# Optimization experiments

Measured on AMD Instinct MI355X. Metric: run time of the kernel, lower is better.

The kernel has to match this reference:

```python
import jax, jax.numpy as jnp
import numpy as np

S = 2048      # words in the sentence
LMAX = 16     # max chars per word (padded)
VOCAB = 50000
ALPHA = 256
CE = 256      # char_embedding_dim (also char-LSTM hidden)
WE = 512      # word_embedding_dim
H = 1024      # hidden_dim of word LSTM


def setup_inputs() -> dict:
    key = jax.random.key(0)
    ks = jax.random.split(key, 13)
    def u(k, shape, scale):
        return jax.random.uniform(k, shape, jnp.float32, -scale, scale)
    sc_c = 1.0 / np.sqrt(CE).astype(np.float32)   # torch LSTM init scale
    sc_w = 1.0 / np.sqrt(H).astype(np.float32)
    return {
        "word_idxs": jax.random.randint(ks[0], (S,), 0, VOCAB),
        "char_idxs": jax.random.randint(ks[1], (S, LMAX), 0, ALPHA),
        "char_lens": jax.random.randint(ks[2], (S,), 1, LMAX + 1),
        "char_emb": jax.random.normal(ks[3], (ALPHA, CE), jnp.float32) * 0.1,
        "word_emb": jax.random.normal(ks[4], (VOCAB, WE), jnp.float32) * 0.1,
        "Wih_c": u(ks[5], (4 * CE, CE), sc_c),
        "Whh_c": u(ks[6], (4 * CE, CE), sc_c),
        "bih_c": u(ks[7], (4 * CE,), sc_c),
        "bhh_c": u(ks[8], (4 * CE,), sc_c),
        "Wih_w": u(ks[9], (4 * H, WE + CE), sc_w),
        "Whh_w": u(ks[10], (4 * H, H), sc_w),
        "bih_w": u(ks[11], (4 * H,), sc_w),
        "bhh_w": u(ks[12], (4 * H,), sc_w),
    }


def _lstm_scan(xs, Wih, Whh, bih, bhh, hdim):
    """Single-layer LSTM, torch gate order (i, f, g, o). xs: [T, B, D] -> hs [T, B, hdim]."""
    B = xs.shape[1]
    bias = bih + bhh
    def step(carry, x):
        h, c = carry
        gates = x @ Wih.T + h @ Whh.T + bias  # [B, 4*hdim]
        i, f, g, o = jnp.split(gates, 4, axis=-1)
        c = jax.nn.sigmoid(f) * c + jax.nn.sigmoid(i) * jnp.tanh(g)
        h = jax.nn.sigmoid(o) * jnp.tanh(c)
        return (h, c), h
    init = (jnp.zeros((B, hdim), xs.dtype), jnp.zeros((B, hdim), xs.dtype))
    _, hs = jax.lax.scan(step, init, xs)
    return hs


def reference(word_idxs, char_idxs, char_lens, char_emb, word_emb,
              Wih_c, Whh_c, bih_c, bhh_c, Wih_w, Whh_w, bih_w, bhh_w):
    # Char LSTM: batch all S words together (fuses the per-word Python loop).
    # Causality makes output at t = len-1 identical to running the true-length seq.
    ce = char_emb[char_idxs]                  # [S, LMAX, CE]
    ce = jnp.swapaxes(ce, 0, 1)               # [LMAX, S, CE] time-major
    hs = _lstm_scan(ce, Wih_c, Whh_c, bih_c, bhh_c, CE)   # [LMAX, S, CE]
    hs = jnp.swapaxes(hs, 0, 1)               # [S, LMAX, CE]
    last = jnp.take_along_axis(hs, (char_lens - 1)[:, None, None], axis=1)[:, 0]  # [S, CE]

    we = word_emb[word_idxs]                  # [S, WE]
    lstm_in = jnp.concatenate([we, last], axis=-1)[:, None, :]  # [S, 1, WE+CE]
    out = _lstm_scan(lstm_in, Wih_w, Whh_w, bih_w, bhh_w, H)    # [S, 1, H]
    # dropout p=0.0 -> identity
    return out
```

## Files before the change

kernel.cpp:

```cpp
#include <hip/hip_runtime.h>
#include <stdint.h>

#define S_WORDS 2048
#define LMAX    16
#define CE      256
#define WE      512
#define HDIM    1024
#define GC      1024
#define GW      4096
#define KW      768
#define NWG_RNN 128
#define NWB_WIN 512
#define NMIR    4
#define RING_U64 (3 * HDIM)

#define IN_GATES_OFF 0
#define LAST_OFF     33554432
#define WT2C_OFF     35651584
#define WT2W_OFF     37748736
#define RING_OFF     WT2C_OFF
#define FLAGS_OFF    (RING_OFF + NMIR * RING_U64 * 8)

typedef float f32x4 __attribute__((ext_vector_type(4)));

#define LD_AGENT(p) __hip_atomic_load((p), __ATOMIC_RELAXED, __HIP_MEMORY_SCOPE_AGENT)

static __device__ __forceinline__ float sigm(float x) { return 1.0f / (1.0f + __expf(-x)); }
static __device__ __forceinline__ float tanh_fast(float x) {
    float ax = fminf(fabsf(x), 15.0f);
    float e  = __expf(2.0f * ax);
    float t  = (e - 1.0f) / (e + 1.0f);
    return copysignf(t, x);
}

__global__ void prep_c_kernel(const float* __restrict__ Wih,
                              const float* __restrict__ Whh,
                              float2* __restrict__ WT2c) {
    int idx = blockIdx.x * blockDim.x + threadIdx.x;
    if (idx >= 256 * GC) return;
    int kp = idx >> 10, row = idx & (GC - 1);
    int k = kp * 2;
    float2 v;
    if (k < CE) { v.x = Wih[row * CE + k];      v.y = Wih[row * CE + k + 1]; }
    else        { v.x = Whh[row * CE + k - CE]; v.y = Whh[row * CE + k - CE + 1]; }
    WT2c[idx] = v;
}

__global__ void prep_w_kernel(const float* __restrict__ Wih,
                              float2* __restrict__ WT2w) {
    int idx = blockIdx.x * blockDim.x + threadIdx.x;
    if (idx >= 384 * GW) return;
    int kp = idx >> 12, row = idx & (GW - 1);
    float2 v;
    v.x = Wih[row * KW + 2 * kp];
    v.y = Wih[row * KW + 2 * kp + 1];
    WT2w[idx] = v;
}

__global__ void __launch_bounds__(256) char_lstm_kernel(
    const int* __restrict__ char_idxs,
    const int* __restrict__ char_lens,
    const float* __restrict__ char_emb,
    const float* __restrict__ bih,
    const float* __restrict__ bhh,
    const float2* __restrict__ WT2c,
    float* __restrict__ last_out)
{
    __shared__ float xh[8][2 * CE];
    const int j = threadIdx.x;
    const int wbase = blockIdx.x * 8;

    float bias[4];
    #pragma unroll
    for (int g = 0; g < 4; g++) bias[g] = bih[g * CE + j] + bhh[g * CE + j];

    int len[8];
    float c[8];
    #pragma unroll
    for (int w = 0; w < 8; w++) {
        c[w] = 0.0f;
        xh[w][CE + j] = 0.0f;
        len[w] = char_lens[wbase + w];
    }

    for (int t = 0; t < LMAX; t++) {
        #pragma unroll
        for (int w = 0; w < 8; w++) {
            int ci = char_idxs[(wbase + w) * LMAX + t];
            xh[w][j] = char_emb[ci * CE + j];
        }
        __syncthreads();

        float acc[4][8];
        #pragma unroll
        for (int g = 0; g < 4; g++)
            #pragma unroll
            for (int w = 0; w < 8; w++) acc[g][w] = 0.0f;

        for (int kp = 0; kp < CE; kp++) {
            float2 wv[4];
            #pragma unroll
            for (int g = 0; g < 4; g++) wv[g] = WT2c[kp * GC + g * CE + j];
            #pragma unroll
            for (int w = 0; w < 8; w++) {
                float2 xv = *(const float2*)&xh[w][2 * kp];
                #pragma unroll
                for (int g = 0; g < 4; g++)
                    acc[g][w] = fmaf(wv[g].y, xv.y, fmaf(wv[g].x, xv.x, acc[g][w]));
            }
        }
        __syncthreads();

        #pragma unroll
        for (int w = 0; w < 8; w++) {
            float iv = sigm(acc[0][w] + bias[0]);
            float fv = sigm(acc[1][w] + bias[1]);
            float gv = tanhf(acc[2][w] + bias[2]);
            float ov = sigm(acc[3][w] + bias[3]);
            c[w] = fv * c[w] + iv * gv;
            float h = ov * tanhf(c[w]);
            xh[w][CE + j] = h;
            if (t == len[w] - 1) last_out[(wbase + w) * CE + j] = h;
        }
    }
}

__global__ void __launch_bounds__(512, 2) fused_word_kernel(
    const float* __restrict__ Whh,
    const int* __restrict__ word_idxs,
    const float* __restrict__ word_emb,
    const float* __restrict__ last,
    const float2* __restrict__ WT2w,
    const float* __restrict__ bih,
    const float* __restrict__ bhh,
    float* __restrict__ in_gates,
    unsigned long long* __restrict__ ring,
    unsigned int* __restrict__ flags,
    float* __restrict__ out)
{
    __shared__ float smem[8 * KW];
    const int tid = threadIdx.x;

    if (blockIdx.x >= NWG_RNN) {
        const int nb    = blockIdx.x - NWG_RNN;
        const int grp   = nb >> 1;
        const int half  = nb & 1;
        const int jj    = tid & 255;
        const int gh    = tid >> 8;
        const int rb2   = half * 2 + gh;
        const int wbase = grp * 8;
        float (*xh)[KW] = (float(*)[KW])smem;

        for (int w = 0; w < 8; w++) {
            int wi = word_idxs[wbase + w];
            xh[w][tid] = word_emb[(size_t)wi * WE + tid];
            if (tid < 256) xh[w][WE + tid] = last[(wbase + w) * CE + tid];
        }
        __syncthreads();

        float acc[4][8];
        #pragma unroll
        for (int g = 0; g < 4; g++)
            #pragma unroll
            for (int w = 0; w < 8; w++) acc[g][w] = 0.0f;

        for (int kp = 0; kp < KW / 2; kp++) {
            float2 wv[4];
            #pragma unroll
            for (int g = 0; g < 4; g++) wv[g] = WT2w[(size_t)kp * GW + rb2 * GC + g * CE + jj];
            #pragma unroll
            for (int w = 0; w < 8; w++) {
                float2 xv = *(const float2*)&xh[w][2 * kp];
                #pragma unroll
                for (int g = 0; g < 4; g++)
                    acc[g][w] = fmaf(wv[g].y, xv.y, fmaf(wv[g].x, xv.x, acc[g][w]));
            }
        }

        #pragma unroll
        for (int g = 0; g < 4; g++) {
            int row = rb2 * GC + g * CE + jj;
            float bias = bih[row] + bhh[row];
            #pragma unroll
            for (int w = 0; w < 8; w++)
                __hip_atomic_store(in_gates + (size_t)(wbase + w) * GW + row,
                                   acc[g][w] + bias,
                                   __ATOMIC_RELAXED, __HIP_MEMORY_SCOPE_AGENT);
        }
        __syncthreads();
        if (tid == 0)
            __hip_atomic_fetch_add(flags + grp, 1u,
                                   __ATOMIC_RELEASE, __HIP_MEMORY_SCOPE_AGENT);
        return;
    }

    const int v = tid >> 6;
    const int l = tid & 63;
    const int unit = blockIdx.x * 8 + v;
    float (*hbb)[HDIM] = (float(*)[HDIM])smem;
    const unsigned long long* ring_my = ring + (size_t)(blockIdx.x & (NMIR - 1)) * RING_U64;

    f32x4 w[4][4];
    #pragma unroll
    for (int g = 0; g < 4; g++)
        #pragma unroll
        for (int cc = 0; cc < 4; cc++)
            w[g][cc] = *(const f32x4*)(Whh + (size_t)(g * HDIM + unit) * HDIM
                                       + cc * 256 + l * 4);
    #pragma unroll
    for (int g = 0; g < 4; g++)
        #pragma unroll
        for (int cc = 0; cc < 4; cc++)
            asm volatile("" : "+v"(w[g][cc]));

    float c_reg = 0.0f;

    for (int t = 0; t < S_WORDS; t++) {
        if ((t & 7) == 0) {
            const unsigned int* fl = flags + (t >> 3);
            while (LD_AGENT(fl) < 2u) {}
        }

        float ing0 = 0.f, ing1 = 0.f, ing2 = 0.f, ing3 = 0.f;
        if (l < 4) {
            const float* ig = in_gates + (size_t)t * GW + unit;
            ing0 = LD_AGENT(ig + 0 * HDIM);
            ing1 = LD_AGENT(ig + 1 * HDIM);
            ing2 = LD_AGENT(ig + 2 * HDIM);
            ing3 = LD_AGENT(ig + 3 * HDIM);
        }

        const unsigned long long* slot = ring_my + (size_t)(t % 3) * HDIM + v * 128;
        unsigned long long a0 = 0, a1 = 0;
        bool ok0 = false, ok1 = false;
        do {
            if (!ok0) {
                a0 = LD_AGENT(slot + l);
                ok0 = ((unsigned)(a0 >> 32) == (unsigned)t);
            }
            if (!ok1) {
                a1 = LD_AGENT(slot + 64 + l);
                ok1 = ((unsigned)(a1 >> 32) == (unsigned)t);
            }
        } while (!__all(ok0 && ok1));
        {
            union { unsigned u32; float f; } c0, c1;
            c0.u32 = (unsigned)a0; c1.u32 = (unsigned)a1;
            hbb[t & 1][v * 128 + l]      = c0.f;
            hbb[t & 1][v * 128 + 64 + l] = c1.f;
        }
        __syncthreads();

        float acc0 = 0.f, acc1 = 0.f, acc2 = 0.f, acc3 = 0.f;
        const float* hb = hbb[t & 1];
        #pragma unroll
        for (int cc = 0; cc < 4; cc++) {
            f32x4 hv = *(const f32x4*)&hb[cc * 256 + l * 4];
            #pragma unroll
            for (int e = 0; e < 4; e++) {
                acc0 = fmaf(w[0][cc][e], hv[e], acc0);
                acc1 = fmaf(w[1][cc][e], hv[e], acc1);
                acc2 = fmaf(w[2][cc][e], hv[e], acc2);
                acc3 = fmaf(w[3][cc][e], hv[e], acc3);
            }
        }
        #pragma unroll
        for (int off = 32; off >= 1; off >>= 1) {
            acc0 += __shfl_xor(acc0, off, 64);
            acc1 += __shfl_xor(acc1, off, 64);
            acc2 += __shfl_xor(acc2, off, 64);
            acc3 += __shfl_xor(acc3, off, 64);
        }

        if (l < 4) {
            float iv = sigm(acc0 + ing0);
            float fv = sigm(acc1 + ing1);
            float gv = tanh_fast(acc2 + ing2);
            float ov = sigm(acc3 + ing3);
            c_reg = fv * c_reg + iv * gv;
            float h = ov * tanh_fast(c_reg);
            union { float f; unsigned u32; } cv; cv.f = h;
            unsigned long long pv =
                ((unsigned long long)(unsigned)(t + 1) << 32) | (unsigned long long)cv.u32;
            __hip_atomic_store(ring + (size_t)l * RING_U64
                                    + (size_t)((t + 1) % 3) * HDIM + unit, pv,
                               __ATOMIC_RELAXED, __HIP_MEMORY_SCOPE_AGENT);
            if (l == 0) out[(size_t)t * HDIM + unit] = h;
        }
    }
}

extern "C" void kernel_launch(void* const* d_in, const int* in_sizes, int n_in,
                              void* d_out, int out_size, void* d_ws, size_t ws_size,
                              hipStream_t stream) {
    const int* word_idxs = (const int*)d_in[0];
    const int* char_idxs = (const int*)d_in[1];
    const int* char_lens = (const int*)d_in[2];
    const float* char_emb = (const float*)d_in[3];
    const float* word_emb = (const float*)d_in[4];
    const float* Wih_c = (const float*)d_in[5];
    const float* Whh_c = (const float*)d_in[6];
    const float* bih_c = (const float*)d_in[7];
    const float* bhh_c = (const float*)d_in[8];
    const float* Wih_w = (const float*)d_in[9];
    const float* Whh_w = (const float*)d_in[10];
    const float* bih_w = (const float*)d_in[11];
    const float* bhh_w = (const float*)d_in[12];

    char* ws = (char*)d_ws;
    float*  in_gates = (float*)(ws + IN_GATES_OFF);
    float*  last     = (float*)(ws + LAST_OFF);
    float2* WT2c     = (float2*)(ws + WT2C_OFF);
    float2* WT2w     = (float2*)(ws + WT2W_OFF);
    unsigned long long* ring = (unsigned long long*)(ws + RING_OFF);
    unsigned int* flags      = (unsigned int*)(ws + FLAGS_OFF);

    hipLaunchKernelGGL(prep_c_kernel, dim3(1024), dim3(256), 0, stream,
                       Wih_c, Whh_c, WT2c);
    hipLaunchKernelGGL(prep_w_kernel, dim3(6144), dim3(256), 0, stream,
                       Wih_w, WT2w);
    hipLaunchKernelGGL(char_lstm_kernel, dim3(256), dim3(256), 0, stream,
                       char_idxs, char_lens, char_emb, bih_c, bhh_c, WT2c, last);
    hipMemsetAsync(ws + RING_OFF, 0,
                   NMIR * RING_U64 * sizeof(unsigned long long) + 256 * sizeof(unsigned int),
                   stream);
    hipLaunchKernelGGL(fused_word_kernel, dim3(NWG_RNN + NWB_WIN), dim3(512), 0, stream,
                       Whh_w, word_idxs, word_emb, last, WT2w, bih_w, bhh_w,
                       in_gates, ring, flags, (float*)d_out);
}
```

Baseline: 5.548 ms.

## Fuse char LSTM into persistent word kernel with flag-based dataflow

Folds the char-LSTM kernel into the persistent word-LSTM launch as an extra group of 256 blocks. Per-group flags let input-projection blocks start as soon as their words' char states exist, so the recurrent chain starts earlier and char work overlaps it. The char blocks now use 512 threads split across gate pairs, and stop at the longest word in their group instead of always running 16 steps. The risks are more spin-wait coordination, a larger shared-memory footprint, and added latency from sleeps in the recurrent wait loop.

```diff
diff --git a/kernel.cpp b/kernel.cpp
--- a/kernel.cpp
+++ b/kernel.cpp
@@ -9,17 +9,21 @@
 #define GC      1024
 #define GW      4096
 #define KW      768
-#define NWG_RNN 128
-#define NWB_WIN 512
+#define NWG_RNN  128
+#define NWB_CHAR 256
+#define NWB_WIN  512
 #define NMIR    4
 #define RING_U64 (3 * HDIM)
 
 #define IN_GATES_OFF 0
+#define WT2C_OFF     31457280
 #define LAST_OFF     33554432
-#define WT2C_OFF     35651584
+#define RING_OFF     35651584
+#define FLAGSW_OFF   (RING_OFF + NMIR * RING_U64 * 8)
+#define FLAGSC_OFF   (FLAGSW_OFF + 1024)
+#define CALL_OFF     (FLAGSC_OFF + 1024)
+#define CTRL_BYTES   (NMIR * RING_U64 * 8 + 1024 + 1024 + 128)
 #define WT2W_OFF     37748736
-#define RING_OFF     WT2C_OFF
-#define FLAGS_OFF    (RING_OFF + NMIR * RING_U64 * 8)
 
 typedef float f32x4 __attribute__((ext_vector_type(4)));
 
@@ -57,92 +61,32 @@
     WT2w[idx] = v;
 }
 
-__global__ void __launch_bounds__(256) char_lstm_kernel(
+__global__ void __launch_bounds__(512, 2) mega_kernel(
+    const int* __restrict__ word_idxs,
     const int* __restrict__ char_idxs,
     const int* __restrict__ char_lens,
     const float* __restrict__ char_emb,
-    const float* __restrict__ bih,
-    const float* __restrict__ bhh,
+    const float* __restrict__ word_emb,
+    const float* __restrict__ bih_c,
+    const float* __restrict__ bhh_c,
+    const float* __restrict__ Whh_w,
+    const float* __restrict__ bih_w,
+    const float* __restrict__ bhh_w,
     const float2* __restrict__ WT2c,
-    float* __restrict__ last_out)
-{
-    __shared__ float xh[8][2 * CE];
-    const int j = threadIdx.x;
-    const int wbase = blockIdx.x * 8;
-
-    float bias[4];
-    #pragma unroll
-    for (int g = 0; g < 4; g++) bias[g] = bih[g * CE + j] + bhh[g * CE + j];
-
-    int len[8];
-    float c[8];
-    #pragma unroll
-    for (int w = 0; w < 8; w++) {
-        c[w] = 0.0f;
-        xh[w][CE + j] = 0.0f;
-        len[w] = char_lens[wbase + w];
-    }
-
-    for (int t = 0; t < LMAX; t++) {
-        #pragma unroll
-        for (int w = 0; w < 8; w++) {
-            int ci = char_idxs[(wbase + w) * LMAX + t];
-            xh[w][j] = char_emb[ci * CE + j];
-        }
-        __syncthreads();
-
-        float acc[4][8];
-        #pragma unroll
-        for (int g = 0; g < 4; g++)
-            #pragma unroll
-            for (int w = 0; w < 8; w++) acc[g][w] = 0.0f;
-
-        for (int kp = 0; kp < CE; kp++) {
-            float2 wv[4];
-            #pragma unroll
-            for (int g = 0; g < 4; g++) wv[g] = WT2c[kp * GC + g * CE + j];
-            #pragma unroll
-            for (int w = 0; w < 8; w++) {
-                float2 xv = *(const float2*)&xh[w][2 * kp];
-                #pragma unroll
-                for (int g = 0; g < 4; g++)
-                    acc[g][w] = fmaf(wv[g].y, xv.y, fmaf(wv[g].x, xv.x, acc[g][w]));
-            }
-        }
-        __syncthreads();
-
-        #pragma unroll
-        for (int w = 0; w < 8; w++) {
-            float iv = sigm(acc[0][w] + bias[0]);
-            float fv = sigm(acc[1][w] + bias[1]);
-            float gv = tanhf(acc[2][w] + bias[2]);
-            float ov = sigm(acc[3][w] + bias[3]);
-            c[w] = fv * c[w] + iv * gv;
-            float h = ov * tanhf(c[w]);
-            xh[w][CE + j] = h;
-            if (t == len[w] - 1) last_out[(wbase + w) * CE + j] = h;
-        }
-    }
-}
-
-__global__ void __launch_bounds__(512, 2) fused_word_kernel(
-    const float* __restrict__ Whh,
-    const int* __restrict__ word_idxs,
-    const float* __restrict__ word_emb,
-    const float* __restrict__ last,
     const float2* __restrict__ WT2w,
-    const float* __restrict__ bih,
-    const float* __restrict__ bhh,
+    float* __restrict__ last,
     float* __restrict__ in_gates,
     unsigned long long* __restrict__ ring,
-    unsigned int* __restrict__ flags,
+    unsigned int* __restrict__ flagsW,
+    unsigned int* __restrict__ flagsC,
+    unsigned int* __restrict__ char_all,
     float* __restrict__ out)
 {
-    __shared__ float smem[8 * KW];
+    __shared__ float smem[13312];
     const int tid = threadIdx.x;
 
-    if (blockIdx.x >= NWG_RNN) {
-        const int nb    = blockIdx.x - NWG_RNN;
+    if (blockIdx.x >= NWG_RNN + NWB_CHAR) {
+        const int nb    = blockIdx.x - (NWG_RNN + NWB_CHAR);
         const int grp   = nb >> 1;
         const int half  = nb & 1;
         const int jj    = tid & 255;
@@ -151,6 +95,13 @@
         const int wbase = grp * 8;
         float (*xh)[KW] = (float(*)[KW])smem;
 
+        if (tid == 0) {
+            while (LD_AGENT(flagsC + grp) < 1u) { __builtin_amdgcn_s_sleep(2); }
+            if (grp >= 240)
+                while (LD_AGENT(char_all) < (unsigned)NWB_CHAR) { __builtin_amdgcn_s_sleep(2); }
+        }
+        __syncthreads();
+
         for (int w = 0; w < 8; w++) {
             int wi = word_idxs[wbase + w];
             xh[w][tid] = word_emb[(size_t)wi * WE + tid];
@@ -180,7 +131,7 @@
         #pragma unroll
         for (int g = 0; g < 4; g++) {
             int row = rb2 * GC + g * CE + jj;
-            float bias = bih[row] + bhh[row];
+            float bias = bih_w[row] + bhh_w[row];
             #pragma unroll
             for (int w = 0; w < 8; w++)
                 __hip_atomic_store(in_gates + (size_t)(wbase + w) * GW + row,
@@ -189,8 +140,97 @@
         }
         __syncthreads();
         if (tid == 0)
-            __hip_atomic_fetch_add(flags + grp, 1u,
+            __hip_atomic_fetch_add(flagsW + grp, 1u,
                                    __ATOMIC_RELEASE, __HIP_MEMORY_SCOPE_AGENT);
+        return;
+    }
+
+    if (blockIdx.x >= NWG_RNN) {
+        const int cb = blockIdx.x - NWG_RNN;
+        const int wbase = cb * 8;
+        const int j = tid & 255;
+        const int p = tid >> 8;
+        float (*cxh)[2 * CE]  = (float(*)[2 * CE])smem;
+        float (*cgex)[256][9] = (float(*)[256][9])(smem + 8 * 2 * CE);
+
+        const float bias0 = bih_c[(2 * p) * CE + j]     + bhh_c[(2 * p) * CE + j];
+        const float bias1 = bih_c[(2 * p + 1) * CE + j] + bhh_c[(2 * p + 1) * CE + j];
+
+        int len[4];
+        float c[4] = {0.f, 0.f, 0.f, 0.f};
+        #pragma unroll
+        for (int ww = 0; ww < 4; ww++) len[ww] = char_lens[wbase + 4 * p + ww];
+        int tmax = 1;
+        #pragma unroll
+        for (int w = 0; w < 8; w++) {
+            int lw = char_lens[wbase + w];
+            tmax = lw > tmax ? lw : tmax;
+        }
+        #pragma unroll
+        for (int ww = 0; ww < 4; ww++) cxh[4 * p + ww][CE + j] = 0.0f;
+
+        const float2* __restrict__ wrow0 = WT2c + (2 * p) * CE + j;
+        const float2* __restrict__ wrow1 = WT2c + (2 * p + 1) * CE + j;
+
+        for (int t = 0; t < tmax; t++) {
+            #pragma unroll
+            for (int ww = 0; ww < 4; ww++) {
+                int w = 4 * p + ww;
+                int ci = char_idxs[(wbase + w) * LMAX + t];
+                cxh[w][j] = char_emb[ci * CE + j];
+            }
+            __syncthreads();
+
+            float a0[8], a1[8];
+            #pragma unroll
+            for (int w = 0; w < 8; w++) { a0[w] = 0.0f; a1[w] = 0.0f; }
+
+            #pragma unroll 2
+            for (int kp = 0; kp < CE; kp++) {
+                float2 wv0 = wrow0[(size_t)kp * GC];
+                float2 wv1 = wrow1[(size_t)kp * GC];
+                #pragma unroll
+                for (int w = 0; w < 8; w++) {
+                    float2 xv = *(const float2*)&cxh[w][2 * kp];
+                    a0[w] = fmaf(wv0.y, xv.y, fmaf(wv0.x, xv.x, a0[w]));
+                    a1[w] = fmaf(wv1.y, xv.y, fmaf(wv1.x, xv.x, a1[w]));
+                }
+            }
+
+            #pragma unroll
+            for (int w = 0; w < 8; w++) {
+                cgex[2 * p][j][w]     = a0[w] + bias0;
+                cgex[2 * p + 1][j][w] = a1[w] + bias1;
+            }
+            __syncthreads();
+
+            #pragma unroll
+            for (int ww = 0; ww < 4; ww++) {
+                int w = 4 * p + ww;
+                float gi = cgex[0][j][w];
+                float gf = cgex[1][j][w];
+                float gg = cgex[2][j][w];
+                float go = cgex[3][j][w];
+                float iv = sigm(gi);
+                float fv = sigm(gf);
+                float gv = tanhf(gg);
+                float ov = sigm(go);
+                c[ww] = fv * c[ww] + iv * gv;
+                float h = ov * tanhf(c[ww]);
+                cxh[w][CE + j] = h;
+                if (t == len[ww] - 1)
+                    __hip_atomic_store(last + (wbase + w) * CE + j, h,
+                                       __ATOMIC_RELAXED, __HIP_MEMORY_SCOPE_AGENT);
+            }
+        }
+
+        __syncthreads();
+        if (tid == 0) {
+            __hip_atomic_fetch_add(flagsC + cb, 1u,
+                                   __ATOMIC_RELEASE, __HIP_MEMORY_SCOPE_AGENT);
+            __hip_atomic_fetch_add(char_all, 1u,
+                                   __ATOMIC_RELEASE, __HIP_MEMORY_SCOPE_AGENT);
+        }
         return;
     }
 
@@ -205,7 +245,7 @@
     for (int g = 0; g < 4; g++)
         #pragma unroll
         for (int cc = 0; cc < 4; cc++)
-            w[g][cc] = *(const f32x4*)(Whh + (size_t)(g * HDIM + unit) * HDIM
+            w[g][cc] = *(const f32x4*)(Whh_w + (size_t)(g * HDIM + unit) * HDIM
                                        + cc * 256 + l * 4);
     #pragma unroll
     for (int g = 0; g < 4; g++)
@@ -217,8 +257,8 @@
 
     for (int t = 0; t < S_WORDS; t++) {
         if ((t & 7) == 0) {
-            const unsigned int* fl = flags + (t >> 3);
-            while (LD_AGENT(fl) < 2u) {}
+            const unsigned int* fl = flagsW + (t >> 3);
+            while (LD_AGENT(fl) < 2u) { __builtin_amdgcn_s_sleep(8); }
         }
 
         float ing0 = 0.f, ing1 = 0.f, ing2 = 0.f, ing3 = 0.f;
@@ -309,22 +349,23 @@
 
     char* ws = (char*)d_ws;
     float*  in_gates = (float*)(ws + IN_GATES_OFF);
+    float2* WT2c     = (float2*)(ws + WT2C_OFF);
     float*  last     = (float*)(ws + LAST_OFF);
-    float2* WT2c     = (float2*)(ws + WT2C_OFF);
     float2* WT2w     = (float2*)(ws + WT2W_OFF);
     unsigned long long* ring = (unsigned long long*)(ws + RING_OFF);
-    unsigned int* flags      = (unsigned int*)(ws + FLAGS_OFF);
+    unsigned int* flagsW     = (unsigned int*)(ws + FLAGSW_OFF);
+    unsigned int* flagsC     = (unsigned int*)(ws + FLAGSC_OFF);
+    unsigned int* char_all   = (unsigned int*)(ws + CALL_OFF);
 
     hipLaunchKernelGGL(prep_c_kernel, dim3(1024), dim3(256), 0, stream,
                        Wih_c, Whh_c, WT2c);
     hipLaunchKernelGGL(prep_w_kernel, dim3(6144), dim3(256), 0, stream,
                        Wih_w, WT2w);
-    hipLaunchKernelGGL(char_lstm_kernel, dim3(256), dim3(256), 0, stream,
-                       char_idxs, char_lens, char_emb, bih_c, bhh_c, WT2c, last);
-    hipMemsetAsync(ws + RING_OFF, 0,
-                   NMIR * RING_U64 * sizeof(unsigned long long) + 256 * sizeof(unsigned int),
-                   stream);
-    hipLaunchKernelGGL(fused_word_kernel, dim3(NWG_RNN + NWB_WIN), dim3(512), 0, stream,
-                       Whh_w, word_idxs, word_emb, last, WT2w, bih_w, bhh_w,
-                       in_gates, ring, flags, (float*)d_out);
-}
+    hipMemsetAsync(ws + RING_OFF, 0, CTRL_BYTES, stream);
+    hipLaunchKernelGGL(mega_kernel, dim3(NWG_RNN + NWB_CHAR + NWB_WIN), dim3(512),
+                       0, stream,
+                       word_idxs, char_idxs, char_lens, char_emb, word_emb,
+                       bih_c, bhh_c, Whh_w, bih_w, bhh_w,
+                       WT2c, WT2w, last, in_gates,
+                       ring, flagsW, flagsC, char_all, (float*)d_out);
+}
```

After: 5.359 ms. 1.04x faster.
